# Kernel tuning notes

Hardware: AMD Instinct MI355X
Metric: run time of the kernel (lower is better)

The kernel has to match this reference:

```python
import jax, jax.numpy as jnp
import numpy as np

B, T, C = 4, 2048, 2048
H, KV, HD = 16, 4, 128  # n_head, n_kv_head, head_dim
G = H // KV             # query heads per kv head


def _rope(t, cos, sin):
    # t: [B, T, h, HD]; cos/sin: [T, HD//2] -> broadcast as [1, T, 1, HD//2]
    tr = t.reshape(t.shape[:-1] + (HD // 2, 2))
    t_r, t_i = tr[..., 0], tr[..., 1]
    c = cos[None, :, None, :]
    s = sin[None, :, None, :]
    o_r = t_r * c - t_i * s
    o_i = t_r * s + t_i * c
    return jnp.stack((o_r, o_i), axis=-1).reshape(t.shape)


def setup_inputs() -> dict:
    key = jax.random.key(0)
    ks = jax.random.split(key, 7)
    sc = 0.02
    return {
        "x": jax.random.normal(ks[0], (B, T, C), jnp.float32),
        "cos_freqs": jnp.cos(jnp.outer(jnp.arange(T, dtype=jnp.float32),
                                       1.0 / (10000.0 ** (jnp.arange(HD // 2, dtype=jnp.float32) * 2 / HD)))),
        "sin_freqs": jnp.sin(jnp.outer(jnp.arange(T, dtype=jnp.float32),
                                       1.0 / (10000.0 ** (jnp.arange(HD // 2, dtype=jnp.float32) * 2 / HD)))),
        "wq": jax.random.normal(ks[1], (H * HD, C), jnp.float32) * sc,
        "wk": jax.random.normal(ks[2], (KV * HD, C), jnp.float32) * sc,
        "wv": jax.random.normal(ks[3], (KV * HD, C), jnp.float32) * sc,
        "wo": jax.random.normal(ks[4], (C, H * HD), jnp.float32) * sc,
    }


def reference(x, cos_freqs, sin_freqs, wq, wk, wv, wo):
    # projections (Linear with bias=False: y = x @ W.T)
    q = (x @ wq.T).reshape(B, T, H, HD)
    k = (x @ wk.T).reshape(B, T, KV, HD)
    v = (x @ wv.T).reshape(B, T, KV, HD)
    q, k = _rope(q, cos_freqs, sin_freqs), _rope(k, cos_freqs, sin_freqs)
    # GQA attention without materializing repeated K/V: group q heads per kv head
    qg = q.reshape(B, T, KV, G, HD).transpose(0, 2, 3, 1, 4)  # [B,KV,G,T,HD]
    kh = k.transpose(0, 2, 1, 3)                              # [B,KV,T,HD]
    vh = v.transpose(0, 2, 1, 3)                              # [B,KV,T,HD]
    scale = 1.0 / jnp.sqrt(jnp.float32(HD))
    scores = jnp.einsum('bkgtd,bksd->bkgts', qg, kh) * scale  # [B,KV,G,T,T]
    mask = jnp.tril(jnp.ones((T, T), dtype=bool))
    scores = jnp.where(mask, scores, jnp.float32(-jnp.inf))
    attn = jax.nn.softmax(scores, axis=-1)
    out = jnp.einsum('bkgts,bksd->bkgtd', attn, vh)           # [B,KV,G,T,HD]
    out = out.transpose(0, 3, 1, 2, 4).reshape(B, T, H * HD)
    return out @ wo.T
```

## Files before the change

kernel.cpp:

```cpp
#include <hip/hip_runtime.h>
#include <hip/hip_bf16.h>
#include <math.h>

typedef __attribute__((ext_vector_type(8))) short short8;
typedef __attribute__((ext_vector_type(4))) float floatx4;

__device__ __forceinline__ float bf2f(unsigned short u) {
  union { unsigned int i; float f; } x; x.i = ((unsigned int)u) << 16; return x.f;
}
__device__ __forceinline__ unsigned short f2bf(float f) {
  union { float f; unsigned int i; } x; x.f = f;
  unsigned int r = x.i + 0x7FFFu + ((x.i >> 16) & 1u);
  return (unsigned short)(r >> 16);
}
__device__ __forceinline__ unsigned int pack2bf(float a, float b) {
  return (unsigned int)f2bf(a) | ((unsigned int)f2bf(b) << 16);
}
__device__ __forceinline__ void gl16(const void* g, void* l) {
  __builtin_amdgcn_global_load_lds(
      (const __attribute__((address_space(1))) unsigned int*)g,
      (__attribute__((address_space(3))) unsigned int*)l, 16, 0, 0);
}

__global__ void cvt_f32_bf16(const float* __restrict__ in, unsigned short* __restrict__ out, int n4) {
  int i = blockIdx.x * blockDim.x + threadIdx.x;
  if (i >= n4) return;
  float4 v = ((const float4*)in)[i];
  ushort4 o;
  o.x = f2bf(v.x); o.y = f2bf(v.y); o.z = f2bf(v.z); o.w = f2bf(v.w);
  ((ushort4*)out)[i] = o;
}

template<int MODE>
__global__ __launch_bounds__(512, 2) void gemm_bt(const unsigned short* __restrict__ A,
                                                  const unsigned short* __restrict__ Bw,
                                                  void* __restrict__ out0,
                                                  unsigned short* __restrict__ vtg,
                                                  const float* __restrict__ cosf,
                                                  const float* __restrict__ sinf,
                                                  int M, int N, int K, int nbx) {
  extern __shared__ unsigned short SM[];
  const int nb = gridDim.x;
  const int bid = blockIdx.x;
  const int tile = (bid & 7) * (nb >> 3) + (bid >> 3);
  const int n0 = (tile % nbx) * 256, m0 = (tile / nbx) * 256;
  const int tid = threadIdx.x;
  const int lane = tid & 63, wave = tid >> 6;
  const int wm = wave >> 2, wn = wave & 3;
  const int r = lane & 15, g = lane >> 4;
  const int rh = r >> 1;
  const int slot = (((r & 1) << 2) | g) ^ rh;

  const int sg8 = (tid & 7) ^ ((tid >> 3) & 7);
  const int srow = 2 * (tid >> 3) + (sg8 >> 2);
  const int scol = (sg8 & 3) * 8;
  const unsigned short* Agb = A  + (size_t)(m0 + srow) * K + scol;
  const unsigned short* Bgb = Bw + (size_t)(n0 + srow) * K + scol;
  const size_t K128 = (size_t)K * 128;
  char* const SMb = (char*)SM;

  const int aob = (wm * 64 + rh) * 64 + slot * 8;
  const int bob = 16384 + (wn * 32 + rh) * 64 + slot * 8;

  auto STA = [&](int s, int t, int kh) {
    const unsigned short* gp = Agb + ((size_t)t << 6) + kh * 32;
    char* d = SMb + s * 65536 + kh * 16384 + wave * 1024;
    gl16(gp,        d);
    gl16(gp + K128, d + 8192);
  };
  auto STB = [&](int s, int t, int kh) {
    const unsigned short* gp = Bgb + ((size_t)t << 6) + kh * 32;
    char* d = SMb + s * 65536 + 32768 + kh * 16384 + wave * 1024;
    gl16(gp,        d);
    gl16(gp + K128, d + 8192);
  };

  floatx4 acc[8][4] = {};
  const int NT = K >> 6;

  STA(0, 0, 0); STB(0, 0, 0);
  STA(0, 0, 1); STB(0, 0, 1);
  asm volatile("s_waitcnt vmcnt(0)" ::: "memory");
  __builtin_amdgcn_s_barrier();
  asm volatile("" ::: "memory");

  short8 bfrA[4], afA[4];
#pragma unroll
  for (int j = 0; j < 4; ++j) bfrA[j] = *(const short8*)&SM[bob + j * 512];
#pragma unroll
  for (int i = 0; i < 4; ++i) afA[i] = *(const short8*)&SM[aob + i * 512];

  for (int t = 0; t < NT; ++t) {
    const int s = t & 1;
    const unsigned short* Ls = SM + s * 32768;
    const unsigned short* Ln = SM + (s ^ 1) * 32768;
    const bool pf = (t + 1 < NT);
    short8 afB[4], bfrB[4], afA2[4], afB2[4];

#pragma unroll
    for (int i = 0; i < 4; ++i) afB[i] = *(const short8*)&Ls[aob + (4 + i) * 512];
    if (pf) { STA(s ^ 1, t + 1, 0); STB(s ^ 1, t + 1, 0); }
    __builtin_amdgcn_s_setprio(1);
#pragma unroll
    for (int i = 0; i < 4; ++i)
#pragma unroll
      for (int j = 0; j < 4; ++j)
        acc[i][j] = __builtin_amdgcn_mfma_f32_16x16x32_bf16(afA[i], bfrA[j], acc[i][j], 0, 0, 0);
    __builtin_amdgcn_s_setprio(0);

#pragma unroll
    for (int j = 0; j < 4; ++j) bfrB[j] = *(const short8*)&Ls[bob + 8192 + j * 512];
#pragma unroll
    for (int i = 0; i < 4; ++i) afA2[i] = *(const short8*)&Ls[aob + 8192 + i * 512];
    if (pf) { STA(s ^ 1, t + 1, 1); STB(s ^ 1, t + 1, 1); }
    __builtin_amdgcn_s_setprio(1);
#pragma unroll
    for (int i = 0; i < 4; ++i)
#pragma unroll
      for (int j = 0; j < 4; ++j)
        acc[4 + i][j] = __builtin_amdgcn_mfma_f32_16x16x32_bf16(afB[i], bfrA[j], acc[4 + i][j], 0, 0, 0);
    __builtin_amdgcn_s_setprio(0);

#pragma unroll
    for (int i = 0; i < 4; ++i) afB2[i] = *(const short8*)&Ls[aob + 8192 + (4 + i) * 512];
    __builtin_amdgcn_s_setprio(1);
#pragma unroll
    for (int i = 0; i < 4; ++i)
#pragma unroll
      for (int j = 0; j < 4; ++j)
        acc[i][j] = __builtin_amdgcn_mfma_f32_16x16x32_bf16(afA2[i], bfrB[j], acc[i][j], 0, 0, 0);
    __builtin_amdgcn_s_setprio(0);

    asm volatile("s_waitcnt lgkmcnt(0)" ::: "memory");
    if (pf) asm volatile("s_waitcnt vmcnt(0)" ::: "memory");
    __builtin_amdgcn_s_barrier();
    asm volatile("" ::: "memory");
    if (pf) {
#pragma unroll
      for (int j = 0; j < 4; ++j) bfrA[j] = *(const short8*)&Ln[bob + j * 512];
#pragma unroll
      for (int i = 0; i < 4; ++i) afA[i] = *(const short8*)&Ln[aob + i * 512];
    }
    __builtin_amdgcn_s_setprio(1);
#pragma unroll
    for (int i = 0; i < 4; ++i)
#pragma unroll
      for (int j = 0; j < 4; ++j)
        acc[4 + i][j] = __builtin_amdgcn_mfma_f32_16x16x32_bf16(afB2[i], bfrB[j], acc[4 + i][j], 0, 0, 0);
    __builtin_amdgcn_s_setprio(0);
  }

  if (MODE == 0) {
    float* SMf = (float*)SM;
    float* outp = (float*)out0;
#pragma unroll
    for (int sp = 0; sp < 4; ++sp) {
      __syncthreads();
      if (wn == sp) {
#pragma unroll
        for (int i = 0; i < 8; ++i)
#pragma unroll
          for (int j = 0; j < 4; ++j)
#pragma unroll
            for (int q = 0; q < 4; ++q)
              SMf[(wm * 128 + i * 16 + g * 4 + q) * 64 + j * 16 + r] = acc[i][j][q];
      }
      __syncthreads();
#pragma unroll
      for (int it = 0; it < 8; ++it) {
        int c = it * 512 + tid;
        int ml = c >> 4, c4 = c & 15;
        float4 v = *(float4*)&SMf[ml * 64 + c4 * 4];
        *(float4*)(outp + (size_t)(m0 + ml) * N + n0 + sp * 64 + c4 * 4) = v;
      }
    }
  } else if (n0 < 2560) {
    unsigned short* outp = (unsigned short*)out0;
    const float scale = (n0 < 2048) ? 0.08838834764831845f : 1.0f;
#pragma unroll
    for (int sp = 0; sp < 2; ++sp) {
      __syncthreads();
      if (wm == sp) {
#pragma unroll
        for (int i = 0; i < 8; ++i)
#pragma unroll
          for (int j = 0; j < 4; ++j)
#pragma unroll
            for (int q = 0; q < 4; ++q)
              SM[(i * 16 + g * 4 + q) * 256 + wn * 64 + j * 16 + r] = f2bf(acc[i][j][q]);
      }
      __syncthreads();
#pragma unroll
      for (int it = 0; it < 8; ++it) {
        int c = it * 512 + tid;
        int ml = c >> 5, c8 = c & 31;
        union { short8 s; unsigned short u[8]; } v;
        v.s = *(short8*)&SM[ml * 256 + c8 * 8];
        const int row = m0 + sp * 128 + ml;
        const int tpos = row & 2047;
        const int d8 = ((n0 + c8 * 8) & 127) >> 3;
        float4 cc = *(const float4*)(cosf + (size_t)tpos * 64 + d8 * 4);
        float4 ss = *(const float4*)(sinf + (size_t)tpos * 64 + d8 * 4);
        float cv[4] = {cc.x, cc.y, cc.z, cc.w};
        float sv[4] = {ss.x, ss.y, ss.z, ss.w};
#pragma unroll
        for (int jj = 0; jj < 4; ++jj) {
          float tr = bf2f(v.u[2 * jj]);
          float ti = bf2f(v.u[2 * jj + 1]);
          float orr = (tr * cv[jj] - ti * sv[jj]) * scale;
          float oi  = (tr * sv[jj] + ti * cv[jj]) * scale;
          v.u[2 * jj]     = f2bf(orr);
          v.u[2 * jj + 1] = f2bf(oi);
        }
        *(short8*)(outp + (size_t)row * N + n0 + c8 * 8) = v.s;
      }
    }
  } else {
#pragma unroll
    for (int sp = 0; sp < 8; ++sp) {
      __syncthreads();
      if (wave == sp) {
#pragma unroll
        for (int i = 0; i < 8; ++i)
#pragma unroll
          for (int j = 0; j < 4; ++j)
#pragma unroll
            for (int q = 0; q < 4; ++q) {
              int ml = i * 16 + g * 4 + q;
              int nl = j * 16 + r;
              SM[nl * 128 + (((ml >> 3) ^ (nl & 7)) << 3) + (ml & 7)] = f2bf(acc[i][j][q]);
            }
      }
      __syncthreads();
#pragma unroll
      for (int it = 0; it < 2; ++it) {
        int c = it * 512 + tid;
        int nl = c >> 4, m8 = c & 15;
        short8 v = *(short8*)&SM[nl * 128 + ((m8 ^ (nl & 7)) << 3)];
        *(short8*)(vtg + (size_t)(n0 - 2560 + (sp & 3) * 64 + nl) * 8192 + m0 + (sp >> 2) * 128 + m8 * 8) = v;
      }
    }
  }
}

__global__ __launch_bounds__(256, 2) void attn_fwd(const unsigned short* __restrict__ QKV,
                                                   const unsigned short* __restrict__ VT,
                                                   unsigned short* __restrict__ O) {
  constexpr int T = 2048;
  constexpr int LDQ = 3072;
  constexpr float NEG = -1e30f;
  __shared__ unsigned short Ks[2][64 * 128];
  __shared__ unsigned short Vs[2][128 * 64];
  const int gid = blockIdx.x;
  const int hb  = gid & 63;
  const int qb  = 15 - (gid >> 6);
  const int h = hb & 15, b = hb >> 4;
  const int kvh = h >> 2;
  const int tid = threadIdx.x, lane = tid & 63, w = tid >> 6;
  const int r = lane & 15, g = lane >> 4;
  const int rbase = (r & 3) + ((r >> 2) << 3);
  const int swzr  = (r & 3) | (((r >> 2) & 1) << 2);
  const size_t bT = (size_t)b * T;

  const unsigned short* Kgb = QKV + bT * LDQ + 2048 + kvh * 128;
  const unsigned short* Vgb = VT + (size_t)(kvh * 128) * 8192 + b * 2048;

  auto STAGE = [&](int bi, int kv0) {
#pragma unroll
    for (int t2 = 0; t2 < 4; ++t2) {
      int ck = w * 4 + t2;
      { int row = ck * 4 + (lane >> 4); int c16 = lane & 15;
        int swz = (row & 3) | (((row >> 3) & 1) << 2);
        gl16(Kgb + (size_t)(kv0 + row) * LDQ + ((c16 ^ swz) << 3),
             (char*)(&Ks[bi][0]) + ck * 1024); }
      { int row = ck * 8 + (lane >> 3); int c16 = lane & 7;
        gl16(Vgb + (size_t)row * 8192 + kv0 + ((c16 ^ (row & 7)) << 3),
             (char*)(&Vs[bi][0]) + ck * 1024); }
    }
  };

  const int q0 = qb * 128;

  short8 qf[2][4];
#pragma unroll
  for (int qt = 0; qt < 2; ++qt) {
    const unsigned short* qp = QKV + (bT + q0 + w * 32 + qt * 16 + r) * LDQ + h * 128;
#pragma unroll
    for (int c = 0; c < 4; ++c) qf[qt][c] = *(const short8*)(qp + c * 32 + g * 8);
  }

  floatx4 acc[8][2] = {};
  float mrun[2] = {NEG, NEG};
  float lrun[2] = {0.f, 0.f};

  const int ntiles = (q0 + 128) >> 6;
  STAGE(0, 0);
  asm volatile("s_waitcnt vmcnt(0)" ::: "memory");
  __syncthreads();

  for (int t = 0; t < ntiles; ++t) {
    const int cur = t & 1;
    const int kv0 = t << 6;
    if (t + 1 < ntiles) STAGE(cur ^ 1, (t + 1) << 6);

    if (kv0 <= q0 + w * 32 + 31) {
      floatx4 st[2][4] = {};
      __builtin_amdgcn_s_setprio(1);
#pragma unroll
      for (int c = 0; c < 4; ++c) {
        short8 kf[4];
#pragma unroll
        for (int kt = 0; kt < 4; ++kt) {
          const int row = rbase + ((kt & 1) << 2) + ((kt >> 1) << 5);
          kf[kt] = *(const short8*)&Ks[cur][row * 128 + (((g + 4 * c) ^ swzr) << 3)];
        }
#pragma unroll
        for (int qt = 0; qt < 2; ++qt)
#pragma unroll
          for (int kt = 0; kt < 4; ++kt)
            st[qt][kt] = __builtin_amdgcn_mfma_f32_16x16x32_bf16(kf[kt], qf[qt][c], st[qt][kt], 0, 0, 0);
      }
      __builtin_amdgcn_s_setprio(0);

      short8 va[2][8];
#pragma unroll
      for (int kc = 0; kc < 2; ++kc)
#pragma unroll
        for (int dt = 0; dt < 8; ++dt)
          va[kc][dt] = *(const short8*)&Vs[cur][(dt * 16 + r) * 64 + (((g + 4 * kc) ^ (r & 7)) << 3)];

#pragma unroll
      for (int qt = 0; qt < 2; ++qt) {
        const int qmin = q0 + w * 32 + qt * 16;
        const int qrow = qmin + r;
        float x[4][4];
        bool needmask = (kv0 + 64 > qmin);
#pragma unroll
        for (int kt = 0; kt < 4; ++kt) {
          const int kvb = kv0 + ((kt >> 1) << 5) + (g << 3) + ((kt & 1) << 2);
#pragma unroll
          for (int j = 0; j < 4; ++j) {
            float v = st[qt][kt][j];
            if (needmask) v = (kvb + j <= qrow) ? v : NEG;
            x[kt][j] = v;
          }
        }
        float mloc = x[0][0];
#pragma unroll
        for (int kt = 0; kt < 4; ++kt)
#pragma unroll
          for (int j = 0; j < 4; ++j) mloc = fmaxf(mloc, x[kt][j]);
        mloc = fmaxf(mloc, __shfl_xor(mloc, 16));
        mloc = fmaxf(mloc, __shfl_xor(mloc, 32));
        if (!__all(mloc <= mrun[qt] + 8.f)) {
          float mnew = fmaxf(mrun[qt], mloc);
          float al = __expf(mrun[qt] - mnew);
          mrun[qt] = mnew;
          lrun[qt] *= al;
#pragma unroll
          for (int dt = 0; dt < 8; ++dt) acc[dt][qt] *= al;
        }
        float pr[4][4], ssum = 0.f;
#pragma unroll
        for (int kt = 0; kt < 4; ++kt)
#pragma unroll
          for (int j = 0; j < 4; ++j) { pr[kt][j] = __expf(x[kt][j] - mrun[qt]); ssum += pr[kt][j]; }
        ssum += __shfl_xor(ssum, 16);
        ssum += __shfl_xor(ssum, 32);
        lrun[qt] += ssum;
        uint2 pk[4];
#pragma unroll
        for (int kt = 0; kt < 4; ++kt) {
          pk[kt].x = pack2bf(pr[kt][0], pr[kt][1]);
          pk[kt].y = pack2bf(pr[kt][2], pr[kt][3]);
        }
        __builtin_amdgcn_s_setprio(1);
#pragma unroll
        for (int kc = 0; kc < 2; ++kc) {
          union { unsigned int u[4]; short8 s; } bw;
          bw.u[0] = pk[2 * kc].x;
          bw.u[1] = pk[2 * kc].y;
          bw.u[2] = pk[2 * kc + 1].x;
          bw.u[3] = pk[2 * kc + 1].y;
#pragma unroll
          for (int dt = 0; dt < 8; ++dt)
            acc[dt][qt] = __builtin_amdgcn_mfma_f32_16x16x32_bf16(va[kc][dt], bw.s, acc[dt][qt], 0, 0, 0);
        }
        __builtin_amdgcn_s_setprio(0);
      }
    }

    asm volatile("s_waitcnt vmcnt(0)" ::: "memory");
    __syncthreads();
  }

#pragma unroll
  for (int qt = 0; qt < 2; ++qt) {
    float inv = 1.f / lrun[qt];
    unsigned short* op = O + (bT + q0 + w * 32 + qt * 16 + r) * 2048 + h * 128;
#pragma unroll
    for (int dt = 0; dt < 8; ++dt) {
      uint2 pkd;
      pkd.x = pack2bf(acc[dt][qt][0] * inv, acc[dt][qt][1] * inv);
      pkd.y = pack2bf(acc[dt][qt][2] * inv, acc[dt][qt][3] * inv);
      *(uint2*)(op + dt * 16 + g * 4) = pkd;
    }
  }
}

extern "C" void kernel_launch(void* const* d_in, const int* in_sizes, int n_in,
                              void* d_out, int out_size, void* d_ws, size_t ws_size,
                              hipStream_t stream) {
  const float* x    = (const float*)d_in[0];
  const float* cosf = (const float*)d_in[1];
  const float* sinf = (const float*)d_in[2];
  const float* wq   = (const float*)d_in[3];
  const float* wk   = (const float*)d_in[4];
  const float* wv   = (const float*)d_in[5];
  const float* wo   = (const float*)d_in[6];

  unsigned short* xb   = (unsigned short*)d_ws;
  unsigned short* qkvw = xb   + 16777216;
  unsigned short* wob  = qkvw + 6291456;
  unsigned short* qkv  = wob  + 4194304;
  unsigned short* Vtg  = qkv  + 25165824;
  unsigned short* AO   = Vtg  + 4194304;

  static int _attr_once = []() {
    hipFuncSetAttribute((const void*)gemm_bt<0>, hipFuncAttributeMaxDynamicSharedMemorySize, 131072);
    hipFuncSetAttribute((const void*)gemm_bt<1>, hipFuncAttributeMaxDynamicSharedMemorySize, 131072);
    return 0;
  }();
  (void)_attr_once;

  cvt_f32_bf16<<<16384, 256, 0, stream>>>(x,  xb,  4194304);
  cvt_f32_bf16<<<4096,  256, 0, stream>>>(wq, qkvw,           1048576);
  cvt_f32_bf16<<<1024,  256, 0, stream>>>(wk, qkvw + 4194304, 262144);
  cvt_f32_bf16<<<1024,  256, 0, stream>>>(wv, qkvw + 5242880, 262144);
  cvt_f32_bf16<<<4096,  256, 0, stream>>>(wo, wob, 1048576);

  gemm_bt<1><<<384, 512, 131072, stream>>>(xb, qkvw, qkv, Vtg, cosf, sinf, 8192, 3072, 2048, 12);

  attn_fwd<<<1024, 256, 0, stream>>>(qkv, Vtg, AO);

  gemm_bt<0><<<256, 512, 131072, stream>>>(AO, wob, d_out, nullptr, nullptr, nullptr, 8192, 2048, 2048, 8);
}
```

Before: 345.4 us.

## Single-buffer V tile in LDS, prefetching next V after register load

Drops the double buffer for V in shared memory, keeping only K double-buffered. Each iteration loads the V fragments into registers, waits on LDS, runs a barrier, then issues the async load of the next V tile into the same buffer. This cuts LDS use per block from 64KB to 48KB, which may allow more resident blocks or waves. The cost is an extra barrier per tile, a shorter window to hide the V prefetch, and V fragments that must now be loaded even by waves whose tile is fully masked.

```diff
diff --git a/kernel.cpp b/kernel.cpp
--- a/kernel.cpp
+++ b/kernel.cpp
@@ -250,7 +250,7 @@
   constexpr int LDQ = 3072;
   constexpr float NEG = -1e30f;
   __shared__ unsigned short Ks[2][64 * 128];
-  __shared__ unsigned short Vs[2][128 * 64];
+  __shared__ unsigned short Vs[128 * 64];
   const int gid = blockIdx.x;
   const int hb  = gid & 63;
   const int qb  = 15 - (gid >> 6);
@@ -265,17 +265,23 @@
   const unsigned short* Kgb = QKV + bT * LDQ + 2048 + kvh * 128;
   const unsigned short* Vgb = VT + (size_t)(kvh * 128) * 8192 + b * 2048;
 
-  auto STAGE = [&](int bi, int kv0) {
+  auto STAGE_K = [&](int bi, int kv0) {
 #pragma unroll
     for (int t2 = 0; t2 < 4; ++t2) {
       int ck = w * 4 + t2;
-      { int row = ck * 4 + (lane >> 4); int c16 = lane & 15;
-        int swz = (row & 3) | (((row >> 3) & 1) << 2);
-        gl16(Kgb + (size_t)(kv0 + row) * LDQ + ((c16 ^ swz) << 3),
-             (char*)(&Ks[bi][0]) + ck * 1024); }
-      { int row = ck * 8 + (lane >> 3); int c16 = lane & 7;
-        gl16(Vgb + (size_t)row * 8192 + kv0 + ((c16 ^ (row & 7)) << 3),
-             (char*)(&Vs[bi][0]) + ck * 1024); }
+      int row = ck * 4 + (lane >> 4); int c16 = lane & 15;
+      int swz = (row & 3) | (((row >> 3) & 1) << 2);
+      gl16(Kgb + (size_t)(kv0 + row) * LDQ + ((c16 ^ swz) << 3),
+           (char*)(&Ks[bi][0]) + ck * 1024);
+    }
+  };
+  auto STAGE_V = [&](int kv0) {
+#pragma unroll
+    for (int t2 = 0; t2 < 4; ++t2) {
+      int ck = w * 4 + t2;
+      int row = ck * 8 + (lane >> 3); int c16 = lane & 7;
+      gl16(Vgb + (size_t)row * 8192 + kv0 + ((c16 ^ (row & 7)) << 3),
+           (char*)(&Vs[0]) + ck * 1024);
     }
   };
 
@@ -294,17 +300,19 @@
   float lrun[2] = {0.f, 0.f};
 
   const int ntiles = (q0 + 128) >> 6;
-  STAGE(0, 0);
+  STAGE_K(0, 0);
+  STAGE_V(0);
   asm volatile("s_waitcnt vmcnt(0)" ::: "memory");
   __syncthreads();
 
   for (int t = 0; t < ntiles; ++t) {
     const int cur = t & 1;
     const int kv0 = t << 6;
-    if (t + 1 < ntiles) STAGE(cur ^ 1, (t + 1) << 6);
-
-    if (kv0 <= q0 + w * 32 + 31) {
-      floatx4 st[2][4] = {};
+    const bool live = (kv0 <= q0 + w * 32 + 31);
+    if (t + 1 < ntiles) STAGE_K(cur ^ 1, (t + 1) << 6);
+
+    floatx4 st[2][4] = {};
+    if (live) {
       __builtin_amdgcn_s_setprio(1);
 #pragma unroll
       for (int c = 0; c < 4; ++c) {
@@ -321,14 +329,21 @@
             st[qt][kt] = __builtin_amdgcn_mfma_f32_16x16x32_bf16(kf[kt], qf[qt][c], st[qt][kt], 0, 0, 0);
       }
       __builtin_amdgcn_s_setprio(0);
-
-      short8 va[2][8];
-#pragma unroll
-      for (int kc = 0; kc < 2; ++kc)
-#pragma unroll
-        for (int dt = 0; dt < 8; ++dt)
-          va[kc][dt] = *(const short8*)&Vs[cur][(dt * 16 + r) * 64 + (((g + 4 * kc) ^ (r & 7)) << 3)];
-
+    }
+
+    short8 va[2][8];
+#pragma unroll
+    for (int kc = 0; kc < 2; ++kc)
+#pragma unroll
+      for (int dt = 0; dt < 8; ++dt)
+        va[kc][dt] = *(const short8*)&Vs[(dt * 16 + r) * 64 + (((g + 4 * kc) ^ (r & 7)) << 3)];
+
+    asm volatile("s_waitcnt lgkmcnt(0)" ::: "memory");
+    __builtin_amdgcn_s_barrier();
+    asm volatile("" ::: "memory");
+    if (t + 1 < ntiles) STAGE_V((t + 1) << 6);
+
+    if (live) {
 #pragma unroll
       for (int qt = 0; qt < 2; ++qt) {
         const int qmin = q0 + w * 32 + qt * 16;
```

Result: no change. 350.5 us (+1.5%).
